# Kernel tuning notes

Measured on AMD Instinct MI355X. Metric: run time of the kernel, lower is better.

## Reference

```python
import jax, jax.numpy as jnp
import numpy as np

NUM_BEAMS = 2


def setup_inputs() -> dict:
    key = jax.random.key(0)
    ks = jax.random.split(key, 5)
    B, T, H, E, F = 128, 32, 768, 4, 3072
    x = jax.random.normal(ks[0], (B, T, H), dtype=jnp.float32)
    Wg = jax.random.normal(ks[1], (E, H), dtype=jnp.float32) * (1.0 / np.sqrt(H))
    W1 = jax.random.normal(ks[2], (E, H, F), dtype=jnp.float32) * (1.0 / np.sqrt(H))
    b1 = jnp.zeros((E, F), dtype=jnp.float32)
    W2 = jax.random.normal(ks[3], (E, F, H), dtype=jnp.float32) * (1.0 / np.sqrt(F))
    b2 = jnp.zeros((E, H), dtype=jnp.float32)
    return {"x": x, "Wg": Wg, "W1": W1, "b1": b1, "W2": W2, "b2": b2}


def reference(x, Wg, W1, b1, W2, b2):
    B, T, H = x.shape
    E = Wg.shape[0]
    nb = NUM_BEAMS
    # ---- forward_gate: mask is all-ones, so masked mean == mean over tokens ----
    x_avg = jnp.mean(x, axis=1)                          # [B, H]
    logits_gate = x_avg @ Wg.T                           # [B, E]
    prob_gate = jax.nn.softmax(logits_gate, axis=-1)     # [B, E]
    # ---- importance auxiliary loss (torch.std uses ddof=1) ----
    importance = jnp.sum(prob_gate, axis=0)              # [E]
    importance_loss = (jnp.std(importance, ddof=1) / jnp.mean(importance)) ** 2
    # ---- beam search, first layer: exp(log(p)) == p, top-k per row ----
    current_scores = jnp.exp(jnp.log(prob_gate))         # == prob_gate (kept for fidelity)
    topk_values, gate_idx = jax.lax.top_k(current_scores, nb)   # [B, nb]
    beam_scores = topk_values.reshape(nb * B)            # row-major flatten, matches .view
    expert_route = gate_idx.reshape(nb * B)[:, None]     # [B*nb, 1]
    beam_idx = jnp.arange(nb * B)
    current_expert_select = expert_route[:, -1]          # [B*nb]
    # ---- first layer: replicate x and scores along beam dim (interleaved) ----
    x_rep = jnp.repeat(x, nb, axis=0)                    # [B*nb, T, H]
    scores_rep = jnp.repeat(prob_gate, nb, axis=0)       # [B*nb, E]
    # input_x = x_rep[beam_idx] is identity here (beam_idx == arange)
    # ---- forward_expert_ffn: run ALL experts, mask+combine with gate prob ----
    h1 = jnp.einsum('bth,ehf->betf', x_rep, W1) + b1[None, :, None, :]
    h1 = jax.nn.gelu(h1, approximate=False)              # torch GELU is exact erf form
    cand = jnp.einsum('betf,efh->beth', h1, W2) + b2[None, :, None, :]  # [B*nb, E, T, H]
    weight = scores_rep * jax.nn.one_hot(current_expert_select, E, dtype=scores_rep.dtype)
    output = jnp.einsum('beth,be->bth', cand, weight)    # weighted sum over experts
    return output, beam_scores, expert_route, beam_idx, importance_loss
```

## Files before the change

### kernel.cpp

```cpp
#include <hip/hip_runtime.h>
#include <math.h>

typedef _Float16 f16;
typedef _Float16 f16x8 __attribute__((ext_vector_type(8)));
typedef float f32x4 __attribute__((ext_vector_type(4)));

#define Bn 128
#define Tn 32
#define Hn 768
#define En 4
#define Fn 3072
#define Rn 256
#define MAXT8 35
#define MAXT4 67

static constexpr size_t OUT_ELEMS  = (size_t)Rn*Tn*Hn;
static constexpr size_t SCORES_OFF = OUT_ELEMS;
static constexpr size_t ROUTE_OFF  = OUT_ELEMS + Rn;
static constexpr size_t BIDX_OFF   = OUT_ELEMS + 2*Rn;
static constexpr size_t LOSS_OFF   = OUT_ELEMS + 3*Rn;

#define WS_WSF    0u
#define WS_ROUTE  4096u
#define WS_GRP    8192u
#define WS_X16    16384u
#define WS_W1T    (WS_X16 + 2u*Bn*Tn*Hn)
#define WS_W2T    (WS_W1T + 2u*En*Hn*Fn)
#define WS_H1     (WS_W2T + 2u*En*Fn*Hn)

#define GLOAD16(g, l) __builtin_amdgcn_global_load_lds( \
    (const __attribute__((address_space(1))) unsigned int*)(g), \
    (__attribute__((address_space(3))) unsigned int*)(l), 16, 0, 0)

__device__ __forceinline__ float fast_gelu(float v) {
  float s = v * 0.70710678118f;
  float a = fabsf(s);
  float t = 1.0f / (1.0f + 0.3275911f * a);
  float y = t*(0.254829592f + t*(-0.284496736f + t*(1.421413741f +
            t*(-1.453152027f + t*1.061405429f))));
  float er = 1.0f - y * __expf(-a*a);
  er = (s < 0.0f) ? -er : er;
  return 0.5f * v * (1.0f + er);
}

__global__ __launch_bounds__(256) void gate_kernel(
    const float* __restrict__ x, const float* __restrict__ Wg,
    float* __restrict__ out, float* __restrict__ wsf, int* __restrict__ route,
    f16* __restrict__ x16)
{
  const int b = blockIdx.x;
  const int tid = threadIdx.x;
  const int w = tid >> 6, l = tid & 63;
  __shared__ float pacc[4][4];
  float a0=0.f, a1=0.f, a2=0.f, a3=0.f;
  const float* xb = x   + (size_t)b*Tn*Hn + (size_t)(w*8)*Hn;
  f16*         xh = x16 + (size_t)b*Tn*Hn + (size_t)(w*8)*Hn;
  #pragma unroll
  for (int k = 0; k < 12; ++k) {
    const int h = l + 64*k;
    const float w0 = Wg[0*Hn+h], w1 = Wg[1*Hn+h], w2 = Wg[2*Hn+h], w3 = Wg[3*Hn+h];
    #pragma unroll
    for (int t = 0; t < 8; ++t) {
      float v = xb[t*Hn + h];
      xh[t*Hn + h] = (f16)v;
      a0 += v*w0; a1 += v*w1; a2 += v*w2; a3 += v*w3;
    }
  }
  #pragma unroll
  for (int o = 32; o > 0; o >>= 1) {
    a0 += __shfl_down(a0,o); a1 += __shfl_down(a1,o);
    a2 += __shfl_down(a2,o); a3 += __shfl_down(a3,o);
  }
  if (l == 0) { pacc[w][0]=a0; pacc[w][1]=a1; pacc[w][2]=a2; pacc[w][3]=a3; }
  __syncthreads();
  if (tid == 0) {
    float lg[4];
    #pragma unroll
    for (int e = 0; e < 4; ++e)
      lg[e] = (pacc[0][e]+pacc[1][e]+pacc[2][e]+pacc[3][e]) * (1.0f/Tn);
    float m = fmaxf(fmaxf(lg[0],lg[1]), fmaxf(lg[2],lg[3]));
    float p[4]; float s = 0.f;
    #pragma unroll
    for (int e = 0; e < 4; ++e) { p[e] = expf(lg[e]-m); s += p[e]; }
    float inv = 1.f/s;
    #pragma unroll
    for (int e = 0; e < 4; ++e) { p[e] *= inv; wsf[b*4+e] = p[e]; }
    int i1 = 0;
    #pragma unroll
    for (int e = 1; e < 4; ++e) if (p[e] > p[i1]) i1 = e;
    int i2 = (i1 == 0) ? 1 : 0;
    #pragma unroll
    for (int e = 0; e < 4; ++e) if (e != i1 && p[e] > p[i2]) i2 = e;
    int idx[2] = {i1, i2};
    #pragma unroll
    for (int k = 0; k < 2; ++k) {
      int r = 2*b + k;
      float pv = p[idx[k]];
      wsf[512 + r] = pv;
      route[r] = idx[k];
      out[SCORES_OFF + r] = pv;
      out[ROUTE_OFF  + r] = (float)idx[k];
      out[BIDX_OFF   + r] = (float)r;
    }
  }
}

__global__ __launch_bounds__(64) void loss_kernel(
    const float* __restrict__ wsf, float* __restrict__ out)
{
  const int l = threadIdx.x;
  float i0=0.f,i1=0.f,i2=0.f,i3=0.f;
  for (int b = l; b < Bn; b += 64) {
    i0 += wsf[b*4+0]; i1 += wsf[b*4+1]; i2 += wsf[b*4+2]; i3 += wsf[b*4+3];
  }
  #pragma unroll
  for (int o = 32; o > 0; o >>= 1) {
    i0 += __shfl_down(i0,o); i1 += __shfl_down(i1,o);
    i2 += __shfl_down(i2,o); i3 += __shfl_down(i3,o);
  }
  if (l == 0) {
    float mean = 0.25f*(i0+i1+i2+i3);
    float d0=i0-mean, d1=i1-mean, d2=i2-mean, d3=i3-mean;
    float var = (d0*d0+d1*d1+d2*d2+d3*d3) * (1.f/3.f);
    out[LOSS_OFF] = var / (mean*mean);
  }
}

__global__ __launch_bounds__(64) void group_kernel(
    const int* __restrict__ route, int* __restrict__ grp)
{
  const int l = threadIdx.x;
  int cnt = 0;
  if (l < 4) { for (int r = 0; r < Rn; ++r) cnt += (route[r] == l); }
  int c0 = __shfl(cnt, 0), c1 = __shfl(cnt, 1), c2 = __shfl(cnt, 2), c3 = __shfl(cnt, 3);
  int off = (l >= 1 ? c0 : 0) + (l >= 2 ? c1 : 0) + (l >= 3 ? c2 : 0);
  if (l < 4) {
    int p = off;
    for (int r = 0; r < Rn; ++r) if (route[r] == l) grp[384 + p++] = r;
  }
  if (l == 0) {
    int cs[4] = {c0, c1, c2, c3};
    int os[4] = {0, c0, c0+c1, c0+c1+c2};
    int nt8 = 0, nt4 = 0;
    for (int e = 0; e < 4; ++e) {
      for (int s = 0; s < cs[e]; s += 8) {
        int nb = cs[e] - s; if (nb > 8) nb = 8;
        grp[8+nt8*3+0] = e; grp[8+nt8*3+1] = os[e]+s; grp[8+nt8*3+2] = nb;
        ++nt8;
      }
      for (int s = 0; s < cs[e]; s += 4) {
        int nb = cs[e] - s; if (nb > 4) nb = 4;
        grp[128+nt4*3+0] = e; grp[128+nt4*3+1] = os[e]+s; grp[128+nt4*3+2] = nb;
        ++nt4;
      }
    }
    grp[0] = nt8;
    grp[1] = nt4;
  }
}

__global__ __launch_bounds__(256) void transcvt_kernel(
    const float* __restrict__ src, f16* __restrict__ dst, int R, int C)
{
  __shared__ f16 t[64][74];
  const int e  = blockIdx.z;
  const int r0 = blockIdx.y*64, c0 = blockIdx.x*64;
  const float* s = src + (size_t)e*R*C;
  f16* d = dst + (size_t)e*R*C;
  const int tid = threadIdx.x;
  const int i  = tid >> 2;
  const int j0 = (tid & 3) * 16;
  #pragma unroll
  for (int q = 0; q < 16; q += 4) {
    float4 v = *(const float4*)(s + (size_t)(r0+i)*C + c0 + j0 + q);
    t[i][j0+q+0]=(f16)v.x; t[i][j0+q+1]=(f16)v.y; t[i][j0+q+2]=(f16)v.z; t[i][j0+q+3]=(f16)v.w;
  }
  __syncthreads();
  f16 o[16];
  #pragma unroll
  for (int q = 0; q < 16; ++q) o[q] = t[j0+q][i];
  *(uint4*)(d + (size_t)(c0+i)*R + r0 + j0)     = *(uint4*)&o[0];
  *(uint4*)(d + (size_t)(c0+i)*R + r0 + j0 + 8) = *(uint4*)&o[8];
}

template<int KD, int ND, int BN, int MI, int NWY, bool G1>
__global__ __launch_bounds__(512, G1 ? 2 : 4) void gemm_kernel(
    const f16* __restrict__ A16, const f16* __restrict__ B16,
    const float* __restrict__ bias, f16* __restrict__ oh,
    float* __restrict__ of, const int* __restrict__ grp,
    const float* __restrict__ wsf)
{
  constexpr int NWM  = 8 / NWY;
  constexpr int BM   = NWM * MI * 16;
  constexpr int NY   = ND / BN;
  constexpr int BI_A = BM / 128;
  constexpr int BI_B = BN / 128;
  constexpr int NLD  = BI_A + BI_B;
  constexpr int BUFSZ = (BM + BN) * 64;
  constexpr int C0   = (MI < 4) ? MI : 4;
  constexpr int TOFF = G1 ? 8 : 128;

  const int ntiles = grp[G1 ? 0 : 1];
  const int tix = blockIdx.x / NY;
  const int ny  = blockIdx.x % NY;
  if (tix >= ntiles) return;
  const int e      = grp[TOFF+tix*3+0];
  const int bstart = grp[TOFF+tix*3+1];
  const int nb     = grp[TOFF+tix*3+2];
  const int n0     = ny * BN;
  const int tid    = threadIdx.x;
  const int lane   = tid & 63;
  const int w      = tid >> 6;

  extern __shared__ __align__(16) char smem[];

  const int srow  = lane >> 2;
  const int sunit = (lane & 3) ^ ((lane >> 3) & 3);
  const f16* asrc[BI_A];
  #pragma unroll
  for (int i = 0; i < BI_A; ++i) {
    int row = (w*BI_A + i)*16 + srow;
    int slot = row >> 5; if (slot >= nb) slot = nb - 1;
    int beam = grp[384 + bstart + slot];
    size_t rbase = G1 ? ((size_t)(beam>>1)*Tn + (row&31)) * (size_t)KD
                      : ((size_t)beam*Tn + (row&31)) * (size_t)KD;
    asrc[i] = A16 + rbase + sunit*8;
  }
  const f16* bsrc[BI_B];
  #pragma unroll
  for (int i = 0; i < BI_B; ++i) {
    int row = (w*BI_B + i)*16 + srow;
    bsrc[i] = B16 + (size_t)e*ND*KD + (size_t)(n0 + row)*KD + sunit*8;
  }

  const int wm = w / NWY, wn = w % NWY;
  const int lr = lane & 15, lk = lane >> 4;
  const int rowA0 = wm*(MI*16);
  const int rowB0 = wn*64;
  const int ub = (lk ^ ((lr >> 1) & 3)) << 4;

  f32x4 acc[MI][4];
  #pragma unroll
  for (int i=0;i<MI;++i)
    #pragma unroll
    for (int j=0;j<4;++j) acc[i][j] = (f32x4){0.f,0.f,0.f,0.f};

  constexpr int NT = KD/32;
  static_assert(NT % 4 == 0 && NT >= 8, "NT must be multiple of 4, >=8");

  auto STAGE = [&](int bsel, int kt2) {
    char* Ad = smem + bsel*BUFSZ + (w*BI_A)*1024;
    #pragma unroll
    for (int i = 0; i < BI_A; ++i) GLOAD16(asrc[i] + kt2*32, Ad + i*1024);
    char* Bd = smem + bsel*BUFSZ + BM*64 + (w*BI_B)*1024;
    #pragma unroll
    for (int i = 0; i < BI_B; ++i) GLOAD16(bsrc[i] + kt2*32, Bd + i*1024);
  };

#define STEP(BUFI, SBI, KTS, VMC, DOST) do { \
    asm volatile("s_waitcnt vmcnt(%0)" :: "i"(VMC) : "memory"); \
    __builtin_amdgcn_sched_barrier(0); \
    __builtin_amdgcn_s_barrier(); \
    __builtin_amdgcn_sched_barrier(0); \
    { \
      const char* Ab = smem + (BUFI)*BUFSZ; \
      const char* Bb = Ab + BM*64; \
      f16x8 af0[C0], bf[4]; \
      _Pragma("unroll") \
      for (int ni=0;ni<4;++ni) \
        bf[ni] = *(const f16x8*)(Bb + (rowB0 + ni*16 + lr)*64 + ub); \
      _Pragma("unroll") \
      for (int mi=0;mi<C0;++mi) \
        af0[mi] = *(const f16x8*)(Ab + (rowA0 + mi*16 + lr)*64 + ub); \
      if (DOST) STAGE(SBI, KTS); \
      __builtin_amdgcn_s_setprio(1); \
      _Pragma("unroll") \
      for (int mi=0;mi<C0;++mi) \
        _Pragma("unroll") \
        for (int ni=0;ni<4;++ni) \
          acc[mi][ni] = __builtin_amdgcn_mfma_f32_16x16x32_f16(af0[mi], bf[ni], acc[mi][ni], 0, 0, 0); \
      __builtin_amdgcn_s_setprio(0); \
      if constexpr (MI == 8) { \
        f16x8 af1[4]; \
        _Pragma("unroll") \
        for (int mi=0;mi<4;++mi) \
          af1[mi] = *(const f16x8*)(Ab + (rowA0 + (mi+4)*16 + lr)*64 + ub); \
        __builtin_amdgcn_s_setprio(1); \
        _Pragma("unroll") \
        for (int mi=0;mi<4;++mi) \
          _Pragma("unroll") \
          for (int ni=0;ni<4;++ni) \
            acc[mi+4][ni] = __builtin_amdgcn_mfma_f32_16x16x32_f16(af1[mi], bf[ni], acc[mi+4][ni], 0, 0, 0); \
        __builtin_amdgcn_s_setprio(0); \
      } \
    } \
  } while (0)

  STAGE(0, 0);
  STAGE(1, 1);
  STAGE(2, 2);

  for (int kt = 0; kt + 8 <= NT; kt += 4) {
    STEP(0, 3, kt+3, 2*NLD, true);
    STEP(1, 0, kt+4, 2*NLD, true);
    STEP(2, 1, kt+5, 2*NLD, true);
    STEP(3, 2, kt+6, 2*NLD, true);
  }
  STEP(0, 3, NT-1, 2*NLD, true);
  STEP(1, 0, 0,    2*NLD, false);
  STEP(2, 0, 0,    NLD,   false);
  STEP(3, 0, 0,    0,     false);
#undef STEP

  __syncthreads();

  const int nvalid = nb * Tn;
  char* cst = smem;
  constexpr int EPH = BM / 128;
  float bvals[4];
  if (G1) {
    #pragma unroll
    for (int ni=0;ni<4;++ni) bvals[ni] = bias[e*ND + n0 + rowB0 + ni*16 + lr];
  }

  #pragma unroll
  for (int h = 0; h < EPH; ++h) {
    #pragma unroll
    for (int mi=0;mi<MI;++mi){
      #pragma unroll
      for (int j=0;j<4;++j){
        const int mglob = rowA0 + mi*16 + (lane>>4)*4 + j;
        if ((mglob >> 7) == h) {
          const int m = mglob & 127;
          const int m7 = m & 7;
          #pragma unroll
          for (int ni=0;ni<4;++ni){
            const int n = rowB0 + ni*16 + lr;
            if (G1) {
              float v = acc[mi][ni][j] + bvals[ni];
              *(f16*)(cst + m*512 + (((n>>3)^m7)<<4) + (n&7)*2) = (f16)fast_gelu(v);
            } else {
              *(float*)(cst + m*512 + (((n>>2)^m7)<<4) + (n&3)*4) = acc[mi][ni][j];
            }
          }
        }
      }
    }
    __syncthreads();
    const int u  = tid & 31;
    const int tr = tid >> 5;
    float4 b4;
    if (!G1) b4 = *(const float4*)(bias + e*ND + n0 + u*4);
    #pragma unroll
    for (int it = 0; it < 8; ++it) {
      const int rl = it*16 + tr;
      const int r  = h*128 + rl;
      if (r < nvalid) {
        const int beam = grp[384 + bstart + (r>>5)];
        if (G1) {
          uint4 v = *(const uint4*)(cst + rl*512 + (((u&24)|((u&7)^(rl&7)))<<4));
          *(uint4*)(oh + ((size_t)beam*Tn + (r&31))*(size_t)ND + n0 + u*8) = v;
        } else {
          const float sc = wsf[512 + beam];
          float4 v = *(const float4*)(cst + rl*512 + (((u&24)|((u&7)^(rl&7)))<<4));
          v.x = (v.x + b4.x)*sc; v.y = (v.y + b4.y)*sc;
          v.z = (v.z + b4.z)*sc; v.w = (v.w + b4.w)*sc;
          *(float4*)(of + ((size_t)beam*Tn + (r&31))*(size_t)Hn + n0 + u*4) = v;
        }
      }
    }
    if (h + 1 < EPH) __syncthreads();
  }
}

extern "C" void kernel_launch(void* const* d_in, const int* in_sizes, int n_in,
                              void* d_out, int out_size, void* d_ws, size_t ws_size,
                              hipStream_t stream)
{
  const float* x  = (const float*)d_in[0];
  const float* Wg = (const float*)d_in[1];
  const float* W1 = (const float*)d_in[2];
  const float* b1 = (const float*)d_in[3];
  const float* W2 = (const float*)d_in[4];
  const float* b2 = (const float*)d_in[5];
  float* out = (float*)d_out;
  char* ws = (char*)d_ws;
  float* wsf  = (float*)(ws + WS_WSF);
  int*   route= (int*)(ws + WS_ROUTE);
  int*   grp  = (int*)(ws + WS_GRP);
  f16*   x16  = (f16*)(ws + WS_X16);
  f16*   w1t  = (f16*)(ws + WS_W1T);
  f16*   w2t  = (f16*)(ws + WS_W2T);
  f16*   h1   = (f16*)(ws + WS_H1);

  gate_kernel<<<Bn, 256, 0, stream>>>(x, Wg, out, wsf, route, x16);
  group_kernel<<<1, 64, 0, stream>>>(route, grp);
  loss_kernel<<<1, 64, 0, stream>>>(wsf, out);
  transcvt_kernel<<<dim3(48,12,4), 256, 0, stream>>>(W1, w1t, Hn, Fn);
  transcvt_kernel<<<dim3(12,48,4), 256, 0, stream>>>(W2, w2t, Fn, Hn);

  auto g1 = gemm_kernel<Hn, Fn, 256, 8, 4, true>;
  auto g2 = gemm_kernel<Fn, Hn, 128, 2, 2, false>;
  const int sm1 = 4 * (256 + 256) * 64;
  const int sm2 = 4 * (128 + 128) * 64;
  hipFuncSetAttribute((const void*)g1, hipFuncAttributeMaxDynamicSharedMemorySize, sm1);
  hipFuncSetAttribute((const void*)g2, hipFuncAttributeMaxDynamicSharedMemorySize, sm2);
  g1<<<MAXT8*12, 512, sm1, stream>>>(x16, w1t, b1, h1, nullptr, grp, wsf);
  g2<<<MAXT4*6,  512, sm2, stream>>>(h1, w2t, b2, nullptr, out, grp, wsf);
}
```

Before: 221.5 us.

## Rewrite expert GEMMs as persistent kernels with 128-row tiles and BK=64 pipeline

Both expert GEMMs now use a uniform 128-row (4-beam) tile list and a persistent grid that statically divides (tile, N-block) jobs across a fixed block count. The K loop moves to 64-wide K steps with 2 or 3 LDS buffers, and each step is split into two MFMA phases. The two weight transpose/convert launches are merged into one. The goal is to remove wasted blocks that exit early on padded tile counts, reduce barrier count per K, and balance work, at the cost of smaller M tiles for GEMM1 (less B reuse) and a different occupancy profile.

```diff
diff --git a/kernel.cpp b/kernel.cpp
--- a/kernel.cpp
+++ b/kernel.cpp
@@ -11,8 +11,6 @@
 #define En 4
 #define Fn 3072
 #define Rn 256
-#define MAXT8 35
-#define MAXT4 67
 
 static constexpr size_t OUT_ELEMS  = (size_t)Rn*Tn*Hn;
 static constexpr size_t SCORES_OFF = OUT_ELEMS;
@@ -141,32 +139,33 @@
   if (l == 0) {
     int cs[4] = {c0, c1, c2, c3};
     int os[4] = {0, c0, c0+c1, c0+c1+c2};
-    int nt8 = 0, nt4 = 0;
+    int nt4 = 0;
     for (int e = 0; e < 4; ++e) {
-      for (int s = 0; s < cs[e]; s += 8) {
-        int nb = cs[e] - s; if (nb > 8) nb = 8;
-        grp[8+nt8*3+0] = e; grp[8+nt8*3+1] = os[e]+s; grp[8+nt8*3+2] = nb;
-        ++nt8;
-      }
       for (int s = 0; s < cs[e]; s += 4) {
         int nb = cs[e] - s; if (nb > 4) nb = 4;
-        grp[128+nt4*3+0] = e; grp[128+nt4*3+1] = os[e]+s; grp[128+nt4*3+2] = nb;
+        grp[8+nt4*3+0] = e; grp[8+nt4*3+1] = os[e]+s; grp[8+nt4*3+2] = nb;
         ++nt4;
       }
     }
-    grp[0] = nt8;
-    grp[1] = nt4;
+    grp[0] = nt4;
   }
 }
 
 __global__ __launch_bounds__(256) void transcvt_kernel(
-    const float* __restrict__ src, f16* __restrict__ dst, int R, int C)
+    const float* __restrict__ W1s, const float* __restrict__ W2s,
+    f16* __restrict__ d1, f16* __restrict__ d2)
 {
   __shared__ f16 t[64][74];
-  const int e  = blockIdx.z;
-  const int r0 = blockIdx.y*64, c0 = blockIdx.x*64;
-  const float* s = src + (size_t)e*R*C;
-  f16* d = dst + (size_t)e*R*C;
+  int bid = blockIdx.x;
+  const float* s; f16* d; int R, C, rc;
+  if (bid < 2304) { s = W1s; d = d1; R = Hn; C = Fn; rc = bid; }
+  else            { s = W2s; d = d2; R = Fn; C = Hn; rc = bid - 2304; }
+  const int e = rc / 576; rc -= e*576;
+  const int nx = C >> 6;
+  const int cy = rc / nx, cx = rc - cy*nx;
+  const int r0 = cy*64, c0 = cx*64;
+  s += (size_t)e*R*C;
+  d += (size_t)e*R*C;
   const int tid = threadIdx.x;
   const int i  = tid >> 2;
   const int j0 = (tid & 3) * 16;
@@ -183,193 +182,201 @@
   *(uint4*)(d + (size_t)(c0+i)*R + r0 + j0 + 8) = *(uint4*)&o[8];
 }
 
-template<int KD, int ND, int BN, int MI, int NWY, bool G1>
-__global__ __launch_bounds__(512, G1 ? 2 : 4) void gemm_kernel(
+template<int KD, int ND, int BN, int NWAVE, int NBUF, bool G1>
+__global__ __launch_bounds__(NWAVE*64, 2) void gemm_kernel(
     const f16* __restrict__ A16, const f16* __restrict__ B16,
     const float* __restrict__ bias, f16* __restrict__ oh,
     float* __restrict__ of, const int* __restrict__ grp,
     const float* __restrict__ wsf)
 {
-  constexpr int NWM  = 8 / NWY;
-  constexpr int BM   = NWM * MI * 16;
+  constexpr int NWY  = BN / 64;
   constexpr int NY   = ND / BN;
-  constexpr int BI_A = BM / 128;
-  constexpr int BI_B = BN / 128;
-  constexpr int NLD  = BI_A + BI_B;
-  constexpr int BUFSZ = (BM + BN) * 64;
-  constexpr int C0   = (MI < 4) ? MI : 4;
-  constexpr int TOFF = G1 ? 8 : 128;
-
-  const int ntiles = grp[G1 ? 0 : 1];
-  const int tix = blockIdx.x / NY;
-  const int ny  = blockIdx.x % NY;
-  if (tix >= ntiles) return;
-  const int e      = grp[TOFF+tix*3+0];
-  const int bstart = grp[TOFF+tix*3+1];
-  const int nb     = grp[TOFF+tix*3+2];
-  const int n0     = ny * BN;
-  const int tid    = threadIdx.x;
-  const int lane   = tid & 63;
-  const int w      = tid >> 6;
+  constexpr int NT   = KD / 64;
+  constexpr int GL_A = 1024 / (NWAVE*64);
+  constexpr int GL_B = (BN*8) / (NWAVE*64);
+  constexpr int NLD  = GL_A + GL_B;
+  constexpr int BUFSZ = (128 + BN) * 128;
+  constexpr int PRE_D = NBUF - 1;
+  constexpr int TPR  = NWAVE*2;
+  static_assert(NT % NBUF == 0, "NT % NBUF");
+
+  const int ntiles = grp[0];
+  const int njobs  = ntiles * NY;
+  const int tid  = threadIdx.x;
+  const int lane = tid & 63;
+  const int w    = tid >> 6;
 
   extern __shared__ __align__(16) char smem[];
-
-  const int srow  = lane >> 2;
-  const int sunit = (lane & 3) ^ ((lane >> 3) & 3);
-  const f16* asrc[BI_A];
-  #pragma unroll
-  for (int i = 0; i < BI_A; ++i) {
-    int row = (w*BI_A + i)*16 + srow;
-    int slot = row >> 5; if (slot >= nb) slot = nb - 1;
-    int beam = grp[384 + bstart + slot];
-    size_t rbase = G1 ? ((size_t)(beam>>1)*Tn + (row&31)) * (size_t)KD
-                      : ((size_t)beam*Tn + (row&31)) * (size_t)KD;
-    asrc[i] = A16 + rbase + sunit*8;
-  }
-  const f16* bsrc[BI_B];
-  #pragma unroll
-  for (int i = 0; i < BI_B; ++i) {
-    int row = (w*BI_B + i)*16 + srow;
-    bsrc[i] = B16 + (size_t)e*ND*KD + (size_t)(n0 + row)*KD + sunit*8;
-  }
 
   const int wm = w / NWY, wn = w % NWY;
   const int lr = lane & 15, lk = lane >> 4;
-  const int rowA0 = wm*(MI*16);
+  const int rowA0 = wm*64;
   const int rowB0 = wn*64;
-  const int ub = (lk ^ ((lr >> 1) & 3)) << 4;
-
-  f32x4 acc[MI][4];
-  #pragma unroll
-  for (int i=0;i<MI;++i)
-    #pragma unroll
-    for (int j=0;j<4;++j) acc[i][j] = (f32x4){0.f,0.f,0.f,0.f};
-
-  constexpr int NT = KD/32;
-  static_assert(NT % 4 == 0 && NT >= 8, "NT must be multiple of 4, >=8");
-
-  auto STAGE = [&](int bsel, int kt2) {
-    char* Ad = smem + bsel*BUFSZ + (w*BI_A)*1024;
-    #pragma unroll
-    for (int i = 0; i < BI_A; ++i) GLOAD16(asrc[i] + kt2*32, Ad + i*1024);
-    char* Bd = smem + bsel*BUFSZ + BM*64 + (w*BI_B)*1024;
-    #pragma unroll
-    for (int i = 0; i < BI_B; ++i) GLOAD16(bsrc[i] + kt2*32, Bd + i*1024);
-  };
-
-#define STEP(BUFI, SBI, KTS, VMC, DOST) do { \
-    asm volatile("s_waitcnt vmcnt(%0)" :: "i"(VMC) : "memory"); \
-    __builtin_amdgcn_sched_barrier(0); \
-    __builtin_amdgcn_s_barrier(); \
-    __builtin_amdgcn_sched_barrier(0); \
-    { \
-      const char* Ab = smem + (BUFI)*BUFSZ; \
-      const char* Bb = Ab + BM*64; \
-      f16x8 af0[C0], bf[4]; \
-      _Pragma("unroll") \
-      for (int ni=0;ni<4;++ni) \
-        bf[ni] = *(const f16x8*)(Bb + (rowB0 + ni*16 + lr)*64 + ub); \
-      _Pragma("unroll") \
-      for (int mi=0;mi<C0;++mi) \
-        af0[mi] = *(const f16x8*)(Ab + (rowA0 + mi*16 + lr)*64 + ub); \
-      if (DOST) STAGE(SBI, KTS); \
-      __builtin_amdgcn_s_setprio(1); \
-      _Pragma("unroll") \
-      for (int mi=0;mi<C0;++mi) \
-        _Pragma("unroll") \
-        for (int ni=0;ni<4;++ni) \
-          acc[mi][ni] = __builtin_amdgcn_mfma_f32_16x16x32_f16(af0[mi], bf[ni], acc[mi][ni], 0, 0, 0); \
-      __builtin_amdgcn_s_setprio(0); \
-      if constexpr (MI == 8) { \
-        f16x8 af1[4]; \
-        _Pragma("unroll") \
-        for (int mi=0;mi<4;++mi) \
-          af1[mi] = *(const f16x8*)(Ab + (rowA0 + (mi+4)*16 + lr)*64 + ub); \
-        __builtin_amdgcn_s_setprio(1); \
-        _Pragma("unroll") \
-        for (int mi=0;mi<4;++mi) \
-          _Pragma("unroll") \
-          for (int ni=0;ni<4;++ni) \
-            acc[mi+4][ni] = __builtin_amdgcn_mfma_f32_16x16x32_f16(af1[mi], bf[ni], acc[mi+4][ni], 0, 0, 0); \
-        __builtin_amdgcn_s_setprio(0); \
-      } \
-    } \
-  } while (0)
-
-  STAGE(0, 0);
-  STAGE(1, 1);
-  STAGE(2, 2);
-
-  for (int kt = 0; kt + 8 <= NT; kt += 4) {
-    STEP(0, 3, kt+3, 2*NLD, true);
-    STEP(1, 0, kt+4, 2*NLD, true);
-    STEP(2, 1, kt+5, 2*NLD, true);
-    STEP(3, 2, kt+6, 2*NLD, true);
-  }
-  STEP(0, 3, NT-1, 2*NLD, true);
-  STEP(1, 0, 0,    2*NLD, false);
-  STEP(2, 0, 0,    NLD,   false);
-  STEP(3, 0, 0,    0,     false);
-#undef STEP
-
-  __syncthreads();
-
-  const int nvalid = nb * Tn;
-  char* cst = smem;
-  constexpr int EPH = BM / 128;
-  float bvals[4];
-  if (G1) {
-    #pragma unroll
-    for (int ni=0;ni<4;++ni) bvals[ni] = bias[e*ND + n0 + rowB0 + ni*16 + lr];
-  }
-
-  #pragma unroll
-  for (int h = 0; h < EPH; ++h) {
-    #pragma unroll
-    for (int mi=0;mi<MI;++mi){
+  const int r7 = lr & 7;
+  const int ub[2] = { ((lk) ^ r7) << 4, ((4+lk) ^ r7) << 4 };
+
+  const int j0 = (int)(((long long)blockIdx.x     * njobs) / gridDim.x);
+  const int j1 = (int)(((long long)(blockIdx.x+1) * njobs) / gridDim.x);
+
+  for (int job = j0; job < j1; ++job) {
+    const int tix = job / NY;
+    const int ny  = job - tix*NY;
+    const int e      = grp[8+tix*3+0];
+    const int bstart = grp[8+tix*3+1];
+    const int nb     = grp[8+tix*3+2];
+    const int n0     = ny * BN;
+
+    const f16* asrc[GL_A];
+    #pragma unroll
+    for (int i = 0; i < GL_A; ++i) {
+      const int U   = (w*GL_A + i)*64 + lane;
+      const int row = U >> 3;
+      const int gu  = (U & 7) ^ (row & 7);
+      int slot = row >> 5; if (slot >= nb) slot = nb - 1;
+      const int beam = grp[384 + bstart + slot];
+      const size_t rbase = (G1 ? (size_t)(beam>>1)*Tn : (size_t)beam*Tn) + (row & 31);
+      asrc[i] = A16 + rbase*(size_t)KD + gu*8;
+    }
+    const f16* bsrc[GL_B];
+    #pragma unroll
+    for (int i = 0; i < GL_B; ++i) {
+      const int U   = (w*GL_B + i)*64 + lane;
+      const int row = U >> 3;
+      const int gu  = (U & 7) ^ (row & 7);
+      bsrc[i] = B16 + (size_t)e*ND*KD + (size_t)(n0 + row)*KD + gu*8;
+    }
+
+    f32x4 acc[4][4];
+    #pragma unroll
+    for (int i=0;i<4;++i)
+      #pragma unroll
+      for (int j=0;j<4;++j) acc[i][j] = (f32x4){0.f,0.f,0.f,0.f};
+
+    auto STAGE = [&](int bsel, int kt2) {
+      char* Ad = smem + bsel*BUFSZ + (w*GL_A)*1024;
+      #pragma unroll
+      for (int i = 0; i < GL_A; ++i) GLOAD16(asrc[i] + kt2*64, Ad + i*1024);
+      char* Bd = smem + bsel*BUFSZ + 128*128 + (w*GL_B)*1024;
+      #pragma unroll
+      for (int i = 0; i < GL_B; ++i) GLOAD16(bsrc[i] + kt2*64, Bd + i*1024);
+    };
+
+#define PHASE(BUFI, KS, PRE, POST) do {                                        \
+      const char* Ab_ = smem + (BUFI)*BUFSZ;                                   \
+      const char* Bb_ = Ab_ + 128*128;                                         \
+      f16x8 af[4], bf[4];                                                      \
+      _Pragma("unroll")                                                        \
+      for (int mi=0;mi<4;++mi)                                                 \
+        af[mi] = *(const f16x8*)(Ab_ + (rowA0+mi*16+lr)*128 + ub[KS]);         \
+      _Pragma("unroll")                                                        \
+      for (int ni=0;ni<4;++ni)                                                 \
+        bf[ni] = *(const f16x8*)(Bb_ + (rowB0+ni*16+lr)*128 + ub[KS]);         \
+      PRE;                                                                     \
+      __builtin_amdgcn_s_barrier();                                            \
+      __builtin_amdgcn_sched_barrier(0);                                       \
+      asm volatile("s_waitcnt lgkmcnt(0)" ::: "memory");                       \
+      __builtin_amdgcn_sched_barrier(0);                                       \
+      __builtin_amdgcn_s_setprio(1);                                           \
+      _Pragma("unroll")                                                        \
+      for (int mi=0;mi<4;++mi)                                                 \
+        _Pragma("unroll")                                                      \
+        for (int ni=0;ni<4;++ni)                                               \
+          acc[mi][ni] = __builtin_amdgcn_mfma_f32_16x16x32_f16(af[mi], bf[ni], acc[mi][ni], 0, 0, 0); \
+      __builtin_amdgcn_s_setprio(0);                                           \
+      POST;                                                                    \
+      __builtin_amdgcn_s_barrier();                                            \
+      __builtin_amdgcn_sched_barrier(0);                                       \
+    } while (0)
+
+#define TILE(BUFI, KT) do {                                                    \
+      PHASE(BUFI, 0,                                                           \
+            { if ((KT)+PRE_D < NT) STAGE(((BUFI)+PRE_D)%NBUF, (KT)+PRE_D); },  \
+            {});                                                               \
+      PHASE(BUFI, 1, {},                                                       \
+            { if (PRE_D == 2 && (KT)+2 < NT) {                                 \
+                asm volatile("s_waitcnt vmcnt(%0)" :: "i"(NLD) : "memory");    \
+              } else if ((KT)+1 < NT) {                                        \
+                asm volatile("s_waitcnt vmcnt(0)" ::: "memory");               \
+              }                                                                \
+              __builtin_amdgcn_sched_barrier(0); });                           \
+    } while (0)
+
+    STAGE(0, 0);
+    if (PRE_D == 2) {
+      STAGE(1, 1);
+      asm volatile("s_waitcnt vmcnt(%0)" :: "i"(NLD) : "memory");
+    } else {
+      asm volatile("s_waitcnt vmcnt(0)" ::: "memory");
+    }
+    __builtin_amdgcn_sched_barrier(0);
+    __builtin_amdgcn_s_barrier();
+    __builtin_amdgcn_sched_barrier(0);
+
+    if constexpr (NBUF == 3) {
+      for (int kt = 0; kt < NT; kt += 3) {
+        TILE(0, kt);
+        TILE(1, kt+1);
+        TILE(2, kt+2);
+      }
+    } else {
+      for (int kt = 0; kt < NT; kt += 2) {
+        TILE(0, kt);
+        TILE(1, kt+1);
+      }
+    }
+#undef TILE
+#undef PHASE
+
+    const int nvalid = nb * Tn;
+    char* cst = smem;
+    float bvals[4];
+    if (G1) {
+      #pragma unroll
+      for (int ni=0;ni<4;++ni) bvals[ni] = bias[e*ND + n0 + rowB0 + ni*16 + lr];
+    }
+    #pragma unroll
+    for (int mi=0;mi<4;++mi){
       #pragma unroll
       for (int j=0;j<4;++j){
-        const int mglob = rowA0 + mi*16 + (lane>>4)*4 + j;
-        if ((mglob >> 7) == h) {
-          const int m = mglob & 127;
-          const int m7 = m & 7;
-          #pragma unroll
-          for (int ni=0;ni<4;++ni){
-            const int n = rowB0 + ni*16 + lr;
-            if (G1) {
-              float v = acc[mi][ni][j] + bvals[ni];
-              *(f16*)(cst + m*512 + (((n>>3)^m7)<<4) + (n&7)*2) = (f16)fast_gelu(v);
-            } else {
-              *(float*)(cst + m*512 + (((n>>2)^m7)<<4) + (n&3)*4) = acc[mi][ni][j];
-            }
+        const int m = rowA0 + mi*16 + (lane>>4)*4 + j;
+        const int m7 = m & 7;
+        #pragma unroll
+        for (int ni=0;ni<4;++ni){
+          const int n = rowB0 + ni*16 + lr;
+          if (G1) {
+            float v = acc[mi][ni][j] + bvals[ni];
+            *(f16*)(cst + m*512 + (((n>>3)^m7)<<4) + (n&7)*2) = (f16)fast_gelu(v);
+          } else {
+            *(float*)(cst + m*512 + (((n>>2)^m7)<<4) + (n&3)*4) = acc[mi][ni][j];
           }
         }
       }
     }
     __syncthreads();
-    const int u  = tid & 31;
-    const int tr = tid >> 5;
-    float4 b4;
-    if (!G1) b4 = *(const float4*)(bias + e*ND + n0 + u*4);
-    #pragma unroll
-    for (int it = 0; it < 8; ++it) {
-      const int rl = it*16 + tr;
-      const int r  = h*128 + rl;
-      if (r < nvalid) {
-        const int beam = grp[384 + bstart + (r>>5)];
-        if (G1) {
-          uint4 v = *(const uint4*)(cst + rl*512 + (((u&24)|((u&7)^(rl&7)))<<4));
-          *(uint4*)(oh + ((size_t)beam*Tn + (r&31))*(size_t)ND + n0 + u*8) = v;
-        } else {
-          const float sc = wsf[512 + beam];
-          float4 v = *(const float4*)(cst + rl*512 + (((u&24)|((u&7)^(rl&7)))<<4));
-          v.x = (v.x + b4.x)*sc; v.y = (v.y + b4.y)*sc;
-          v.z = (v.z + b4.z)*sc; v.w = (v.w + b4.w)*sc;
-          *(float4*)(of + ((size_t)beam*Tn + (r&31))*(size_t)Hn + n0 + u*4) = v;
+    {
+      const int u  = tid & 31;
+      const int tr = tid >> 5;
+      float4 b4;
+      if (!G1) b4 = *(const float4*)(bias + e*ND + n0 + u*4);
+      #pragma unroll
+      for (int it = 0; it < 128/TPR; ++it) {
+        const int rl = it*TPR + tr;
+        if (rl < nvalid) {
+          const int beam = grp[384 + bstart + (rl>>5)];
+          if (G1) {
+            uint4 v = *(const uint4*)(cst + rl*512 + (((u&24)|((u&7)^(rl&7)))<<4));
+            *(uint4*)(oh + ((size_t)beam*Tn + (rl&31))*(size_t)ND + n0 + u*8) = v;
+          } else {
+            const float sc = wsf[512 + beam];
+            float4 v = *(const float4*)(cst + rl*512 + (((u&24)|((u&7)^(rl&7)))<<4));
+            v.x = (v.x + b4.x)*sc; v.y = (v.y + b4.y)*sc;
+            v.z = (v.z + b4.z)*sc; v.w = (v.w + b4.w)*sc;
+            *(float4*)(of + ((size_t)beam*Tn + (rl&31))*(size_t)Hn + n0 + u*4) = v;
+          }
         }
       }
     }
-    if (h + 1 < EPH) __syncthreads();
+    __syncthreads();
   }
 }
 
@@ -396,15 +403,14 @@
   gate_kernel<<<Bn, 256, 0, stream>>>(x, Wg, out, wsf, route, x16);
   group_kernel<<<1, 64, 0, stream>>>(route, grp);
   loss_kernel<<<1, 64, 0, stream>>>(wsf, out);
-  transcvt_kernel<<<dim3(48,12,4), 256, 0, stream>>>(W1, w1t, Hn, Fn);
-  transcvt_kernel<<<dim3(12,48,4), 256, 0, stream>>>(W2, w2t, Fn, Hn);
-
-  auto g1 = gemm_kernel<Hn, Fn, 256, 8, 4, true>;
-  auto g2 = gemm_kernel<Fn, Hn, 128, 2, 2, false>;
-  const int sm1 = 4 * (256 + 256) * 64;
-  const int sm2 = 4 * (128 + 128) * 64;
+  transcvt_kernel<<<4608, 256, 0, stream>>>(W1, W2, w1t, w2t);
+
+  auto g1 = gemm_kernel<Hn, Fn, 256, 8, 3, true>;
+  auto g2 = gemm_kernel<Fn, Hn, 128, 4, 2, false>;
+  const int sm1 = 3 * (128 + 256) * 128;
+  const int sm2 = 2 * (128 + 128) * 128;
   hipFuncSetAttribute((const void*)g1, hipFuncAttributeMaxDynamicSharedMemorySize, sm1);
   hipFuncSetAttribute((const void*)g2, hipFuncAttributeMaxDynamicSharedMemorySize, sm2);
-  g1<<<MAXT8*12, 512, sm1, stream>>>(x16, w1t, b1, h1, nullptr, grp, wsf);
-  g2<<<MAXT4*6,  512, sm2, stream>>>(h1, w2t, b2, nullptr, out, grp, wsf);
-}
+  g1<<<256, 512, sm1, stream>>>(x16, w1t, b1, h1, nullptr, grp, wsf);
+  g2<<<512, 256, sm2, stream>>>(h1, w2t, b2, nullptr, out, grp, wsf);
+}
```

Measured after the change: 231.8 us. 4.7% more time.
